# Kernel tuning notes

Hardware: AMD Instinct MI355X
Metric: run time of the kernel (lower is better)

The kernel has to match this reference:

```python
import jax, jax.numpy as jnp
import numpy as np

EMB = 1024
E = 8        # num_experts
TOPK = 2
HID = 2048   # expert_dim

def setup_inputs() -> dict:
    key = jax.random.key(0)
    ks = jax.random.split(key, 10)
    s = lambda fan_in: 1.0 / np.sqrt(fan_in)
    x  = jax.random.normal(ks[0], (2, 2048, EMB), dtype=jnp.float32)
    Wr = jax.random.normal(ks[1], (EMB, E), dtype=jnp.float32) * s(EMB)
    br = jnp.zeros((E,), dtype=jnp.float32)
    # stacked expert weights, stored (in, out) so y = x @ W + b
    W1 = jax.random.normal(ks[2], (E, EMB, HID), dtype=jnp.float32) * s(EMB)
    b1 = jax.random.normal(ks[3], (E, HID), dtype=jnp.float32) * 0.01
    Wg = jax.random.normal(ks[4], (E, HID, HID), dtype=jnp.float32) * s(HID)
    bg = jax.random.normal(ks[5], (E, HID), dtype=jnp.float32) * 0.01
    W2 = jax.random.normal(ks[6], (E, HID, EMB), dtype=jnp.float32) * s(HID)
    b2 = jax.random.normal(ks[7], (E, EMB), dtype=jnp.float32) * 0.01
    return {"x": x, "Wr": Wr, "br": br, "W1": W1, "b1": b1,
            "Wg": Wg, "bg": bg, "W2": W2, "b2": b2}

def reference(x, Wr, br, W1, b1, Wg, bg, W2, b2):
    B, S, D = x.shape
    xt = x.reshape(B * S, D)                                  # [T, D]
    logits = xt @ Wr + br                                     # [T, E]
    probs = jax.nn.softmax(logits, axis=-1)
    topk_p, topk_i = jax.lax.top_k(probs, TOPK)               # [T, K]
    # dense gate matrix (top-k probs, NOT renormalized, as in source)
    gates = jnp.sum(jax.nn.one_hot(topk_i, E, dtype=xt.dtype) * topk_p[..., None], axis=1)  # [T, E]
    # expert MLP: layer1 (no act) -> relu(linear) -> layer2, for all experts
    h = jnp.einsum('td,edh->teh', xt, W1) + b1                # [T, E, HID]
    h = jax.nn.relu(jnp.einsum('teh,ehg->teg', h, Wg) + bg)   # [T, E, HID]
    y = jnp.einsum('teh,ehd->ted', h, W2) + b2                # [T, E, D]
    out = jnp.einsum('te,ted->td', gates, y)                  # weighted combine
    return out.reshape(B, S, D)
```

## Files before the change

kernel.cpp:

```cpp
#include <hip/hip_runtime.h>
#include <hip/hip_bf16.h>
#include <stdint.h>

#define NTOK 4096
#define EMBD 1024
#define NEXP 8
#define HIDD 2048
#define NPAIR (NTOK * 2)

typedef __attribute__((ext_vector_type(8))) __bf16 bf16x8;
typedef __attribute__((ext_vector_type(4))) float f32x4;

union V16 { uint4 u; bf16x8 b; };

__device__ __forceinline__ uint16_t f2bf(float f) {
    uint32_t u = __float_as_uint(f);
    return (uint16_t)((u + 0x7FFFu + ((u >> 16) & 1u)) >> 16);
}
__device__ __forceinline__ float bf2f(uint16_t u) {
    return __uint_as_float(((uint32_t)u) << 16);
}
__device__ __forceinline__ void gl_lds16(const uint16_t* g, uint16_t* l) {
    __builtin_amdgcn_global_load_lds(
        (const __attribute__((address_space(1))) void*)g,
        (__attribute__((address_space(3))) void*)l, 16, 0, 0);
}

__global__ __launch_bounds__(256) void cast_x_kernel(const float* __restrict__ x,
                                                     uint16_t* __restrict__ xb) {
    int i = blockIdx.x * 256 + threadIdx.x;
    float4 v = ((const float4*)x)[i];
    ushort4 o;
    o.x = f2bf(v.x); o.y = f2bf(v.y); o.z = f2bf(v.z); o.w = f2bf(v.w);
    ((ushort4*)xb)[i] = o;
}

__global__ __launch_bounds__(256) void transcast_kernel(const float* __restrict__ src,
                                                        uint16_t* __restrict__ dst,
                                                        int K, int N) {
    int e = blockIdx.z;
    int k0 = blockIdx.y * 64, n0 = blockIdx.x * 64;
    __shared__ uint16_t tile[64][65];
    const float* S = src + ((size_t)e * K + k0) * N + n0;
    uint16_t* D = dst + ((size_t)e * N + n0) * K + k0;
    int tx = threadIdx.x & 63, ty = threadIdx.x >> 6;
#pragma unroll
    for (int kk = ty; kk < 64; kk += 4)
        tile[kk][tx] = f2bf(S[(size_t)kk * N + tx]);
    __syncthreads();
    int tx2 = threadIdx.x & 31, tyw = threadIdx.x >> 5;
#pragma unroll
    for (int nn = tyw; nn < 64; nn += 8) {
        uint32_t lo = tile[2 * tx2][nn], hi = tile[2 * tx2 + 1][nn];
        *(uint32_t*)&D[(size_t)nn * K + 2 * tx2] = lo | (hi << 16);
    }
}

__global__ __launch_bounds__(64) void router_kernel(const float* __restrict__ x,
                                                    const float* __restrict__ Wr,
                                                    const float* __restrict__ br,
                                                    int* __restrict__ counts,
                                                    int* __restrict__ pair_e,
                                                    float* __restrict__ pair_p) {
    int tok = blockIdx.x;
    int lane = threadIdx.x;
    const float* xr = x + (size_t)tok * EMBD;
    float acc[NEXP];
#pragma unroll
    for (int e = 0; e < NEXP; e++) acc[e] = 0.f;
    for (int d = lane; d < EMBD; d += 64) {
        float xv = xr[d];
#pragma unroll
        for (int e = 0; e < NEXP; e++) acc[e] += xv * Wr[d * NEXP + e];
    }
#pragma unroll
    for (int e = 0; e < NEXP; e++) {
#pragma unroll
        for (int off = 32; off > 0; off >>= 1)
            acc[e] += __shfl_down(acc[e], off, 64);
    }
    if (lane == 0) {
        float lg[NEXP];
#pragma unroll
        for (int e = 0; e < NEXP; e++) lg[e] = acc[e] + br[e];
        int e0 = 0;
#pragma unroll
        for (int e = 1; e < NEXP; e++) if (lg[e] > lg[e0]) e0 = e;
        int e1 = (e0 == 0) ? 1 : 0;
#pragma unroll
        for (int e = 0; e < NEXP; e++) if (e != e0 && lg[e] > lg[e1]) e1 = e;
        float mx = lg[0];
#pragma unroll
        for (int e = 1; e < NEXP; e++) mx = fmaxf(mx, lg[e]);
        float s = 0.f, p[NEXP];
#pragma unroll
        for (int e = 0; e < NEXP; e++) { p[e] = __expf(lg[e] - mx); s += p[e]; }
        float inv = 1.f / s;
        pair_e[tok * 2 + 0] = e0; pair_p[tok * 2 + 0] = p[e0] * inv;
        pair_e[tok * 2 + 1] = e1; pair_p[tok * 2 + 1] = p[e1] * inv;
        atomicAdd(&counts[e0], 1);
        atomicAdd(&counts[e1], 1);
    }
}

__global__ void scan_kernel(const int* __restrict__ counts, int* __restrict__ offsets) {
    if (threadIdx.x == 0 && blockIdx.x == 0) {
        int s = 0;
        for (int e = 0; e < NEXP; e++) { offsets[e] = s; s += counts[e]; }
    }
}

__global__ __launch_bounds__(256) void scatter_kernel(const int* __restrict__ pair_e,
                                                      const int* __restrict__ offsets,
                                                      int* __restrict__ cursors,
                                                      int* __restrict__ toklist,
                                                      int* __restrict__ posmap) {
    int i = blockIdx.x * 256 + threadIdx.x;
    int e = pair_e[i];
    int pos = offsets[e] + atomicAdd(&cursors[e], 1);
    toklist[pos] = i >> 1;
    posmap[i] = pos;
}

template <int KDIM, int NDIM, bool GATHER_A, bool RELU>
__global__ __launch_bounds__(256) void gemm_kernel(
    const uint16_t* __restrict__ Abase, const uint16_t* __restrict__ Btbase,
    const float* __restrict__ bbase, uint16_t* __restrict__ Out,
    const int* __restrict__ counts, const int* __restrict__ offsets,
    const int* __restrict__ toklist) {
    int e = blockIdx.z;
    int n_e = counts[e];
    int m0 = blockIdx.y * 128;
    if (m0 >= n_e) return;
    int n0 = blockIdx.x * 128;
    int offs = offsets[e];
    const uint16_t* Bt = Btbase + (size_t)e * NDIM * KDIM;

    __shared__ uint16_t As[128 * 32];
    __shared__ uint16_t Bs[128 * 32];

    int tid = threadIdx.x;
    int lane = tid & 63;
    int wave = tid >> 6;

    int sr = tid >> 2;
    int ss = tid & 3;
    const uint16_t* arp[2];
    const uint16_t* brp[2];
#pragma unroll
    for (int p = 0; p < 2; p++) {
        int r = p * 64 + sr;
        int gs = ss ^ ((r >> 1) & 3);
        int grow;
        if (GATHER_A) {
            int idx = m0 + r;
            if (idx >= n_e) idx = 0;
            grow = toklist[offs + idx];
        } else {
            grow = offs + m0 + r;
        }
        arp[p] = Abase + (size_t)grow * KDIM + gs * 8;
        brp[p] = Bt + (size_t)(n0 + r) * KDIM + gs * 8;
    }
    uint16_t* alds[2] = { &As[wave * 512], &As[2048 + wave * 512] };
    uint16_t* blds[2] = { &Bs[wave * 512], &Bs[2048 + wave * 512] };

    int wm = (wave >> 1) * 64;
    int wn = (wave & 1) * 64;
    int l16 = lane & 15, qd = lane >> 4;
    const uint16_t* afp[4];
    const uint16_t* bfp[4];
#pragma unroll
    for (int t = 0; t < 4; t++) {
        int ar = wm + t * 16 + l16;
        afp[t] = &As[ar * 32 + (qd ^ ((ar >> 1) & 3)) * 8];
        int br = wn + t * 16 + l16;
        bfp[t] = &Bs[br * 32 + (qd ^ ((br >> 1) & 3)) * 8];
    }

    f32x4 acc[4][4];
    f32x4 zero = {0.f, 0.f, 0.f, 0.f};
#pragma unroll
    for (int i = 0; i < 4; i++)
#pragma unroll
        for (int j = 0; j < 4; j++) acc[i][j] = zero;

    for (int kb = 0; kb < KDIM; kb += 32) {
#pragma unroll
        for (int p = 0; p < 2; p++) {
            gl_lds16(arp[p] + kb, alds[p]);
            gl_lds16(brp[p] + kb, blds[p]);
        }
        __syncthreads();
        V16 af[4], bf[4];
#pragma unroll
        for (int t = 0; t < 4; t++) {
            af[t].u = *(const uint4*)(afp[t]);
            bf[t].u = *(const uint4*)(bfp[t]);
        }
#pragma unroll
        for (int i = 0; i < 4; i++)
#pragma unroll
            for (int j = 0; j < 4; j++)
                acc[i][j] = __builtin_amdgcn_mfma_f32_16x16x32_bf16(
                    af[i].b, bf[j].b, acc[i][j], 0, 0, 0);
        __syncthreads();
    }

    const float* bias = bbase + (size_t)e * NDIM;
    int mrem = n_e - m0;
#pragma unroll
    for (int i = 0; i < 4; i++) {
        int rb = wm + i * 16 + qd * 4;
#pragma unroll
        for (int j = 0; j < 4; j++) {
            int col = n0 + wn + j * 16 + l16;
            float bv = bias[col];
#pragma unroll
            for (int r = 0; r < 4; r++) {
                int lr = rb + r;
                if (lr < mrem) {
                    float v = acc[i][j][r] + bv;
                    if (RELU) v = fmaxf(v, 0.f);
                    Out[(size_t)(offs + m0 + lr) * NDIM + col] = f2bf(v);
                }
            }
        }
    }
}

__global__ __launch_bounds__(256) void combine_kernel(const uint16_t* __restrict__ y,
                                                      const int* __restrict__ posmap,
                                                      const float* __restrict__ pair_p,
                                                      float* __restrict__ out) {
    int t = blockIdx.x;
    int d4 = threadIdx.x;
    int p0 = posmap[t * 2], p1 = posmap[t * 2 + 1];
    float w0 = pair_p[t * 2], w1 = pair_p[t * 2 + 1];
    ushort4 a = ((const ushort4*)(y + (size_t)p0 * EMBD))[d4];
    ushort4 b = ((const ushort4*)(y + (size_t)p1 * EMBD))[d4];
    float4 o;
    o.x = w0 * bf2f(a.x) + w1 * bf2f(b.x);
    o.y = w0 * bf2f(a.y) + w1 * bf2f(b.y);
    o.z = w0 * bf2f(a.z) + w1 * bf2f(b.z);
    o.w = w0 * bf2f(a.w) + w1 * bf2f(b.w);
    ((float4*)(out + (size_t)t * EMBD))[d4] = o;
}

extern "C" void kernel_launch(void* const* d_in, const int* in_sizes, int n_in,
                              void* d_out, int out_size, void* d_ws, size_t ws_size,
                              hipStream_t stream) {
    const float* x  = (const float*)d_in[0];
    const float* Wr = (const float*)d_in[1];
    const float* br = (const float*)d_in[2];
    const float* W1 = (const float*)d_in[3];
    const float* b1 = (const float*)d_in[4];
    const float* Wg = (const float*)d_in[5];
    const float* bg = (const float*)d_in[6];
    const float* W2 = (const float*)d_in[7];
    const float* b2 = (const float*)d_in[8];
    float* out = (float*)d_out;

    char* ws = (char*)d_ws;
    uint16_t* xb  = (uint16_t*)ws;
    uint16_t* h   = (uint16_t*)(ws + (8ull << 20));
    uint16_t* yb  = h;
    uint16_t* W1t = (uint16_t*)(ws + (40ull << 20));
    uint16_t* g   = W1t;
    uint16_t* Wgt = (uint16_t*)(ws + (72ull << 20));
    uint16_t* W2t = (uint16_t*)(ws + (136ull << 20));
    int* meta = (int*)(ws + (168ull << 20));
    int*   counts  = meta;
    int*   offsets = meta + 8;
    int*   cursors = meta + 16;
    int*   pair_e  = meta + 24;
    int*   toklist = meta + 24 + NPAIR;
    int*   posmap  = meta + 24 + 2 * NPAIR;
    float* pair_p  = (float*)(meta + 24 + 3 * NPAIR);

    hipMemsetAsync(counts, 0, 24 * sizeof(int), stream);

    cast_x_kernel<<<(NTOK * EMBD) / (256 * 4), 256, 0, stream>>>(x, xb);
    transcast_kernel<<<dim3(HIDD / 64, EMBD / 64, NEXP), 256, 0, stream>>>(W1, W1t, EMBD, HIDD);
    transcast_kernel<<<dim3(HIDD / 64, HIDD / 64, NEXP), 256, 0, stream>>>(Wg, Wgt, HIDD, HIDD);
    transcast_kernel<<<dim3(EMBD / 64, HIDD / 64, NEXP), 256, 0, stream>>>(W2, W2t, HIDD, EMBD);
    router_kernel<<<NTOK, 64, 0, stream>>>(x, Wr, br, counts, pair_e, pair_p);
    scan_kernel<<<1, 64, 0, stream>>>(counts, offsets);
    scatter_kernel<<<NPAIR / 256, 256, 0, stream>>>(pair_e, offsets, cursors, toklist, posmap);

    gemm_kernel<EMBD, HIDD, true, false>
        <<<dim3(HIDD / 128, NTOK / 128, NEXP), 256, 0, stream>>>(
            xb, W1t, b1, h, counts, offsets, toklist);
    gemm_kernel<HIDD, HIDD, false, true>
        <<<dim3(HIDD / 128, NTOK / 128, NEXP), 256, 0, stream>>>(
            h, Wgt, bg, g, counts, offsets, toklist);
    gemm_kernel<HIDD, EMBD, false, false>
        <<<dim3(EMBD / 128, NTOK / 128, NEXP), 256, 0, stream>>>(
            g, W2t, b2, yb, counts, offsets, toklist);
    combine_kernel<<<NTOK, 256, 0, stream>>>(yb, posmap, pair_p, out);
}
```

Before: 765.9 us.

## Merge weight transcasts, fold x cast into router, drop scan kernel

Merges the three weight transpose-cast launches into one kernel with a flat tile index, and widens its global reads and writes to float4 and uint4. The bf16 cast of x moves into the router kernel, and the scan kernel is replaced by each consumer summing the expert counts itself. The aim is to cut launch overhead and inefficient narrow memory traffic in the preprocessing phase, which is dominated by converting about 200MB of fp32 weights. In exchange, every GEMM block and scatter thread recomputes the prefix sum, and the router now makes scalar 2-byte stores.

```diff
diff --git a/kernel.cpp b/kernel.cpp
--- a/kernel.cpp
+++ b/kernel.cpp
@@ -26,50 +26,67 @@
         (__attribute__((address_space(3))) void*)l, 16, 0, 0);
 }
 
-__global__ __launch_bounds__(256) void cast_x_kernel(const float* __restrict__ x,
-                                                     uint16_t* __restrict__ xb) {
-    int i = blockIdx.x * 256 + threadIdx.x;
-    float4 v = ((const float4*)x)[i];
-    ushort4 o;
-    o.x = f2bf(v.x); o.y = f2bf(v.y); o.z = f2bf(v.z); o.w = f2bf(v.w);
-    ((ushort4*)xb)[i] = o;
-}
-
-__global__ __launch_bounds__(256) void transcast_kernel(const float* __restrict__ src,
-                                                        uint16_t* __restrict__ dst,
-                                                        int K, int N) {
-    int e = blockIdx.z;
-    int k0 = blockIdx.y * 64, n0 = blockIdx.x * 64;
-    __shared__ uint16_t tile[64][65];
+#define W1_TILES 4096
+#define WG_TILES 8192
+#define W2_TILES 4096
+__global__ __launch_bounds__(256) void transcast3_kernel(
+    const float* __restrict__ W1, const float* __restrict__ Wg,
+    const float* __restrict__ W2, uint16_t* __restrict__ W1t,
+    uint16_t* __restrict__ Wgt, uint16_t* __restrict__ W2t) {
+    int id = blockIdx.x;
+    const float* src; uint16_t* dst; int K, N;
+    if (id < W1_TILES) { src = W1; dst = W1t; K = EMBD; N = HIDD; }
+    else if (id < W1_TILES + WG_TILES) { id -= W1_TILES; src = Wg; dst = Wgt; K = HIDD; N = HIDD; }
+    else { id -= W1_TILES + WG_TILES; src = W2; dst = W2t; K = HIDD; N = EMBD; }
+    int tn = N >> 6, tk = K >> 6;
+    int per_e = tn * tk;
+    int e = id / per_e, r = id % per_e;
+    int n0 = (r % tn) * 64, k0 = (r / tn) * 64;
+
+    __shared__ uint16_t tile[64][68];
     const float* S = src + ((size_t)e * K + k0) * N + n0;
     uint16_t* D = dst + ((size_t)e * N + n0) * K + k0;
-    int tx = threadIdx.x & 63, ty = threadIdx.x >> 6;
-#pragma unroll
-    for (int kk = ty; kk < 64; kk += 4)
-        tile[kk][tx] = f2bf(S[(size_t)kk * N + tx]);
+    int t = threadIdx.x;
+    int rn = (t & 15) * 4, rk = t >> 4;
+#pragma unroll
+    for (int p = 0; p < 4; p++) {
+        int k = rk + p * 16;
+        float4 v = *(const float4*)(S + (size_t)k * N + rn);
+        ushort4 o;
+        o.x = f2bf(v.x); o.y = f2bf(v.y); o.z = f2bf(v.z); o.w = f2bf(v.w);
+        *(ushort4*)&tile[k][rn] = o;
+    }
     __syncthreads();
-    int tx2 = threadIdx.x & 31, tyw = threadIdx.x >> 5;
-#pragma unroll
-    for (int nn = tyw; nn < 64; nn += 8) {
-        uint32_t lo = tile[2 * tx2][nn], hi = tile[2 * tx2 + 1][nn];
-        *(uint32_t*)&D[(size_t)nn * K + 2 * tx2] = lo | (hi << 16);
+    int wn = t >> 3, wk = (t & 7) * 8;
+#pragma unroll
+    for (int p = 0; p < 2; p++) {
+        int n = wn + p * 32;
+        uint32_t w0 = (uint32_t)tile[wk + 0][n] | ((uint32_t)tile[wk + 1][n] << 16);
+        uint32_t w1 = (uint32_t)tile[wk + 2][n] | ((uint32_t)tile[wk + 3][n] << 16);
+        uint32_t w2 = (uint32_t)tile[wk + 4][n] | ((uint32_t)tile[wk + 5][n] << 16);
+        uint32_t w3 = (uint32_t)tile[wk + 6][n] | ((uint32_t)tile[wk + 7][n] << 16);
+        uint4 pk = {w0, w1, w2, w3};
+        *(uint4*)(D + (size_t)n * K + wk) = pk;
     }
 }
 
 __global__ __launch_bounds__(64) void router_kernel(const float* __restrict__ x,
                                                     const float* __restrict__ Wr,
                                                     const float* __restrict__ br,
+                                                    uint16_t* __restrict__ xb,
                                                     int* __restrict__ counts,
                                                     int* __restrict__ pair_e,
                                                     float* __restrict__ pair_p) {
     int tok = blockIdx.x;
     int lane = threadIdx.x;
     const float* xr = x + (size_t)tok * EMBD;
+    uint16_t* xbr = xb + (size_t)tok * EMBD;
     float acc[NEXP];
 #pragma unroll
     for (int e = 0; e < NEXP; e++) acc[e] = 0.f;
     for (int d = lane; d < EMBD; d += 64) {
         float xv = xr[d];
+        xbr[d] = f2bf(xv);
 #pragma unroll
         for (int e = 0; e < NEXP; e++) acc[e] += xv * Wr[d * NEXP + e];
     }
@@ -103,21 +120,16 @@
     }
 }
 
-__global__ void scan_kernel(const int* __restrict__ counts, int* __restrict__ offsets) {
-    if (threadIdx.x == 0 && blockIdx.x == 0) {
-        int s = 0;
-        for (int e = 0; e < NEXP; e++) { offsets[e] = s; s += counts[e]; }
-    }
-}
-
 __global__ __launch_bounds__(256) void scatter_kernel(const int* __restrict__ pair_e,
-                                                      const int* __restrict__ offsets,
+                                                      const int* __restrict__ counts,
                                                       int* __restrict__ cursors,
                                                       int* __restrict__ toklist,
                                                       int* __restrict__ posmap) {
     int i = blockIdx.x * 256 + threadIdx.x;
     int e = pair_e[i];
-    int pos = offsets[e] + atomicAdd(&cursors[e], 1);
+    int offs = 0;
+    for (int j = 0; j < NEXP; j++) offs += (j < e) ? counts[j] : 0;
+    int pos = offs + atomicAdd(&cursors[e], 1);
     toklist[pos] = i >> 1;
     posmap[i] = pos;
 }
@@ -126,14 +138,14 @@
 __global__ __launch_bounds__(256) void gemm_kernel(
     const uint16_t* __restrict__ Abase, const uint16_t* __restrict__ Btbase,
     const float* __restrict__ bbase, uint16_t* __restrict__ Out,
-    const int* __restrict__ counts, const int* __restrict__ offsets,
-    const int* __restrict__ toklist) {
+    const int* __restrict__ counts, const int* __restrict__ toklist) {
     int e = blockIdx.z;
+    int offs = 0;
+    for (int j = 0; j < NEXP; j++) offs += (j < e) ? counts[j] : 0;
     int n_e = counts[e];
     int m0 = blockIdx.y * 128;
     if (m0 >= n_e) return;
     int n0 = blockIdx.x * 128;
-    int offs = offsets[e];
     const uint16_t* Bt = Btbase + (size_t)e * NDIM * KDIM;
 
     __shared__ uint16_t As[128 * 32];
@@ -271,31 +283,27 @@
     uint16_t* W2t = (uint16_t*)(ws + (136ull << 20));
     int* meta = (int*)(ws + (168ull << 20));
     int*   counts  = meta;
-    int*   offsets = meta + 8;
-    int*   cursors = meta + 16;
-    int*   pair_e  = meta + 24;
-    int*   toklist = meta + 24 + NPAIR;
-    int*   posmap  = meta + 24 + 2 * NPAIR;
-    float* pair_p  = (float*)(meta + 24 + 3 * NPAIR);
-
-    hipMemsetAsync(counts, 0, 24 * sizeof(int), stream);
-
-    cast_x_kernel<<<(NTOK * EMBD) / (256 * 4), 256, 0, stream>>>(x, xb);
-    transcast_kernel<<<dim3(HIDD / 64, EMBD / 64, NEXP), 256, 0, stream>>>(W1, W1t, EMBD, HIDD);
-    transcast_kernel<<<dim3(HIDD / 64, HIDD / 64, NEXP), 256, 0, stream>>>(Wg, Wgt, HIDD, HIDD);
-    transcast_kernel<<<dim3(EMBD / 64, HIDD / 64, NEXP), 256, 0, stream>>>(W2, W2t, HIDD, EMBD);
-    router_kernel<<<NTOK, 64, 0, stream>>>(x, Wr, br, counts, pair_e, pair_p);
-    scan_kernel<<<1, 64, 0, stream>>>(counts, offsets);
-    scatter_kernel<<<NPAIR / 256, 256, 0, stream>>>(pair_e, offsets, cursors, toklist, posmap);
+    int*   cursors = meta + 8;
+    int*   pair_e  = meta + 16;
+    int*   toklist = meta + 16 + NPAIR;
+    int*   posmap  = meta + 16 + 2 * NPAIR;
+    float* pair_p  = (float*)(meta + 16 + 3 * NPAIR);
+
+    hipMemsetAsync(counts, 0, 16 * sizeof(int), stream);
+
+    router_kernel<<<NTOK, 64, 0, stream>>>(x, Wr, br, xb, counts, pair_e, pair_p);
+    transcast3_kernel<<<W1_TILES + WG_TILES + W2_TILES, 256, 0, stream>>>(
+        W1, Wg, W2, W1t, Wgt, W2t);
+    scatter_kernel<<<NPAIR / 256, 256, 0, stream>>>(pair_e, counts, cursors, toklist, posmap);
 
     gemm_kernel<EMBD, HIDD, true, false>
         <<<dim3(HIDD / 128, NTOK / 128, NEXP), 256, 0, stream>>>(
-            xb, W1t, b1, h, counts, offsets, toklist);
+            xb, W1t, b1, h, counts, toklist);
     gemm_kernel<HIDD, HIDD, false, true>
         <<<dim3(HIDD / 128, NTOK / 128, NEXP), 256, 0, stream>>>(
-            h, Wgt, bg, g, counts, offsets, toklist);
+            h, Wgt, bg, g, counts, toklist);
     gemm_kernel<HIDD, EMBD, false, false>
         <<<dim3(EMBD / 128, NTOK / 128, NEXP), 256, 0, stream>>>(
-            g, W2t, b2, yb, counts, offsets, toklist);
+            g, W2t, b2, yb, counts, toklist);
     combine_kernel<<<NTOK, 256, 0, stream>>>(yb, posmap, pair_p, out);
 }
```

Result: faster. 737.1 us (-3.7%).
